# Performance work log

Measured on AMD Instinct MI355X. Metric: run time of the kernel, lower is better.

Reference implementation:

```python
import jax, jax.numpy as jnp
import numpy as np

# SGCN (AsynSpiGCN) internals are not in the source; reconstructed as a standard
# LIF spiking-GCN: per time step, spikes propagate along edges weighted by
# edge_attr (gather src -> scatter-add dst), membrane potential decays with
# decay_alpha, neurons fire above threshold unless refractory, reset to v_r.
V_REST = 0.0
V_R = 0.0
SPEED = 1.0
THRESH = 0.5
REFRAC = 2.0
DECAY = 0.8
T_STEPS = 8
BETA = 0.5

N_NODES = 50000
N_EDGES = 800000
IN_DIM = 256
HID_DIM = 128


def setup_inputs() -> dict:
    key = jax.random.key(0)
    k1, k2, k3, k4, k5 = jax.random.split(key, 5)
    x = jax.random.normal(k1, (N_NODES, IN_DIM), dtype=jnp.float32)
    spike_node = jax.random.randint(k2, (N_NODES,), 0, 2, dtype=jnp.int32)
    edge_index = jax.random.randint(k3, (2, N_EDGES), 0, N_NODES, dtype=jnp.int32)
    node_indices = jnp.arange(N_NODES, dtype=jnp.int32)
    edge_attr = jax.random.uniform(k4, (N_EDGES,), dtype=jnp.float32)
    W = jax.random.normal(k5, (IN_DIM, HID_DIM), dtype=jnp.float32) * 0.05
    b = jnp.zeros((HID_DIM,), dtype=jnp.float32)
    return {"x": x, "spike_node": spike_node, "edge_index": edge_index,
            "node_indices": node_indices, "edge_attr": edge_attr, "W": W, "b": b}


def reference(x, spike_node, edge_index, node_indices, edge_attr, W, b):
    N = x.shape[0]
    # Linear projection + per-feature min-max standardization over nodes (dim 0)
    h = x @ W + b
    mn = h.min(axis=0, keepdims=True)
    mx = h.max(axis=0, keepdims=True)
    h = (h - mn) / (mx - mn + 1e-6)

    src, dst = edge_index[0], edge_index[1]
    v0 = jnp.full_like(h, V_REST)            # membrane potential [N, H]
    ref0 = jnp.zeros_like(h)                 # refractory counters [N, H]
    s0 = jnp.broadcast_to(spike_node.astype(h.dtype)[:, None], h.shape)

    def step(carry, _):
        v, ref, s = carry
        msg = s[src] * edge_attr[:, None]                      # [E, H] gather
        agg = jax.ops.segment_sum(msg, dst, num_segments=N)    # [N, H] scatter-add
        v = DECAY * v + SPEED * h + agg
        can_fire = ref <= 0
        spk = ((v >= THRESH) & can_fire).astype(h.dtype)
        v = jnp.where(spk > 0, V_R, v)
        ref = jnp.where(spk > 0, REFRAC, jnp.maximum(ref - 1.0, 0.0))
        return (v, ref, spk), spk

    (vT, _, _), spike_matrix = jax.lax.scan(step, (v0, ref0, s0), None, length=T_STEPS)
    fusion_tensor = h + BETA * vT
    return fusion_tensor, spike_matrix
```

## Files before the change

kernel.cpp:

```cpp
#include <hip/hip_runtime.h>
#include <cstdint>

#define N_NODES 50000
#define N_EDGES 800000
#define IN_DIM  256
#define HID     128
#define T_STEPS 8

static __device__ __forceinline__ unsigned int enc_f(float f) {
    unsigned int u = __float_as_uint(f);
    return (u & 0x80000000u) ? ~u : (u | 0x80000000u);
}
static __device__ __forceinline__ float dec_f(unsigned int u) {
    unsigned int b = (u & 0x80000000u) ? (u ^ 0x80000000u) : ~u;
    return __uint_as_float(b);
}

__global__ void k_count(const int* __restrict__ dst, int* __restrict__ counts) {
    int e = blockIdx.x * blockDim.x + threadIdx.x;
    if (e < N_EDGES) atomicAdd(&counts[dst[e]], 1);
}

__global__ void k_scan1(const int* __restrict__ counts, int* __restrict__ row_tmp,
                        int* __restrict__ blocksum) {
    __shared__ int sh[256];
    int t = threadIdx.x, i = blockIdx.x * 256 + t;
    int c = (i < N_NODES) ? counts[i] : 0;
    sh[t] = c; __syncthreads();
    for (int off = 1; off < 256; off <<= 1) {
        int val = (t >= off) ? sh[t - off] : 0;
        __syncthreads();
        sh[t] += val;
        __syncthreads();
    }
    if (i < N_NODES) row_tmp[i] = sh[t] - c;
    if (t == 255) blocksum[blockIdx.x] = sh[255];
}

__global__ void k_scan2(const int* __restrict__ blocksum, int* __restrict__ blockoff,
                        int nb, int* __restrict__ row_ptr) {
    if (threadIdx.x == 0) {
        int acc = 0;
        for (int b = 0; b < nb; ++b) { blockoff[b] = acc; acc += blocksum[b]; }
        row_ptr[N_NODES] = acc;
    }
}

__global__ void k_scan3(const int* __restrict__ row_tmp, const int* __restrict__ blockoff,
                        int* __restrict__ row_ptr) {
    int i = blockIdx.x * blockDim.x + threadIdx.x;
    if (i < N_NODES) row_ptr[i] = row_tmp[i] + blockoff[i >> 8];
}

__global__ void k_fill(const int* __restrict__ dst, const int* __restrict__ src,
                       const float* __restrict__ attr,
                       const int* __restrict__ row_ptr, int* __restrict__ cursor,
                       int* __restrict__ eid, int2* __restrict__ edata) {
    int e = blockIdx.x * blockDim.x + threadIdx.x;
    if (e >= N_EDGES) return;
    int d = dst[e];
    int p = row_ptr[d] + atomicAdd(&cursor[d], 1);
    eid[p]   = e;
    edata[p] = make_int2(src[e], __float_as_int(attr[e]));
}

__global__ __launch_bounds__(256) void k_bsort(const int* __restrict__ row_ptr,
                                               int* __restrict__ eid,
                                               int2* __restrict__ edata) {
    int node = blockIdx.x * 4 + (threadIdx.x >> 6);
    int l = threadIdx.x & 63;
    int beg = row_ptr[node], end = row_ptr[node + 1], cnt = end - beg;
    if (cnt <= 1) return;
    if (cnt <= 64) {
        int key = 0x7FFFFFFF, sv = 0, av = 0;
        if (l < cnt) { key = eid[beg + l]; int2 d = edata[beg + l]; sv = d.x; av = d.y; }
        #pragma unroll
        for (int k = 2; k <= 64; k <<= 1) {
            for (int j = k >> 1; j > 0; j >>= 1) {
                int pk = __shfl_xor(key, j);
                int ps = __shfl_xor(sv, j);
                int pa = __shfl_xor(av, j);
                bool lower = (l & j) == 0;
                bool asc   = (l & k) == 0;
                bool take_min = (lower == asc);
                bool take = take_min ? (pk < key) : (pk > key);
                if (take) { key = pk; sv = ps; av = pa; }
            }
        }
        if (l < cnt) { eid[beg + l] = key; edata[beg + l] = make_int2(sv, av); }
    } else if (l == 0) {
        for (int i = beg + 1; i < end; ++i) {
            int ke = eid[i]; int2 kd = edata[i];
            int m = i - 1;
            while (m >= beg && eid[m] > ke) {
                eid[m+1] = eid[m]; edata[m+1] = edata[m]; --m;
            }
            eid[m+1] = ke; edata[m+1] = kd;
        }
    }
}

__global__ __launch_bounds__(256) void k_gemm(const float* __restrict__ x,
                                              const float* __restrict__ W,
                                              const float* __restrict__ b,
                                              float* __restrict__ h,
                                              unsigned int* __restrict__ mn_e,
                                              unsigned int* __restrict__ mx_e) {
    __shared__ float Ws[32 * 128];
    __shared__ float xs[64 * 36];
    __shared__ float red_mn[8 * 128];
    __shared__ float red_mx[8 * 128];
    const int tid = threadIdx.x;
    const int n0 = blockIdx.x * 64;
    const int jt = tid & 31, nt = tid >> 5;
    const int j0 = jt * 4;

    float acc[8][4];
    #pragma unroll
    for (int a = 0; a < 8; ++a)
        #pragma unroll
        for (int c = 0; c < 4; ++c) acc[a][c] = 0.0f;

    const int ldn = tid >> 2;
    const int kq  = (tid & 3) * 8;
    const int xrow = (n0 + ldn < N_NODES) ? (n0 + ldn) : (N_NODES - 1);
    const float* xg = x + (size_t)xrow * IN_DIM;

    for (int kc = 0; kc < IN_DIM; kc += 32) {
        __syncthreads();
        float4 xa = *(const float4*)(xg + kc + kq);
        float4 xb = *(const float4*)(xg + kc + kq + 4);
        *(float4*)&xs[ldn * 36 + kq]     = xa;
        *(float4*)&xs[ldn * 36 + kq + 4] = xb;
        #pragma unroll
        for (int p = 0; p < 4; ++p) {
            int r = nt + p * 8;
            *(float4*)&Ws[r * 128 + j0] =
                *(const float4*)(W + (size_t)(kc + r) * HID + j0);
        }
        __syncthreads();
        const float* xbase = &xs[nt * 8 * 36];
        #pragma unroll 4
        for (int k = 0; k < 32; ++k) {
            float4 wf = *(const float4*)&Ws[k * 128 + j0];
            #pragma unroll
            for (int ni = 0; ni < 8; ++ni) {
                float xv = xbase[ni * 36 + k];
                acc[ni][0] = __fmaf_rn(xv, wf.x, acc[ni][0]);
                acc[ni][1] = __fmaf_rn(xv, wf.y, acc[ni][1]);
                acc[ni][2] = __fmaf_rn(xv, wf.z, acc[ni][2]);
                acc[ni][3] = __fmaf_rn(xv, wf.w, acc[ni][3]);
            }
        }
    }

    float4 bv = *(const float4*)(b + j0);
    float lmn[4], lmx[4];
    #pragma unroll
    for (int c = 0; c < 4; ++c) { lmn[c] = INFINITY; lmx[c] = -INFINITY; }
    #pragma unroll
    for (int ni = 0; ni < 8; ++ni) {
        acc[ni][0] = __fadd_rn(acc[ni][0], bv.x);
        acc[ni][1] = __fadd_rn(acc[ni][1], bv.y);
        acc[ni][2] = __fadd_rn(acc[ni][2], bv.z);
        acc[ni][3] = __fadd_rn(acc[ni][3], bv.w);
        #pragma unroll
        for (int c = 0; c < 4; ++c) {
            lmn[c] = fminf(lmn[c], acc[ni][c]);
            lmx[c] = fmaxf(lmx[c], acc[ni][c]);
        }
    }
    #pragma unroll
    for (int c = 0; c < 4; ++c) {
        red_mn[nt * 128 + j0 + c] = lmn[c];
        red_mx[nt * 128 + j0 + c] = lmx[c];
    }
    __syncthreads();
    if (tid < 128) {
        float mnv = red_mn[tid], mxv = red_mx[tid];
        #pragma unroll
        for (int r = 1; r < 8; ++r) {
            mnv = fminf(mnv, red_mn[r * 128 + tid]);
            mxv = fmaxf(mxv, red_mx[r * 128 + tid]);
        }
        atomicMin(&mn_e[tid], enc_f(mnv));
        atomicMax(&mx_e[tid], enc_f(mxv));
    }
    #pragma unroll
    for (int ni = 0; ni < 8; ++ni) {
        int n = n0 + nt * 8 + ni;
        if (n < N_NODES)
            *(float4*)&h[(size_t)n * HID + j0] =
                make_float4(acc[ni][0], acc[ni][1], acc[ni][2], acc[ni][3]);
    }
}

__global__ void k_init_bits(const int* __restrict__ spike_node, uint32_t* __restrict__ sb) {
    int n = blockIdx.x * blockDim.x + threadIdx.x;
    if (n >= N_NODES) return;
    uint32_t f = spike_node[n] ? 0xFFFFFFFFu : 0u;
    sb[(size_t)n * 4 + 0] = f;
    sb[(size_t)n * 4 + 1] = f;
    sb[(size_t)n * 4 + 2] = f;
    sb[(size_t)n * 4 + 3] = f;
}

static __device__ __forceinline__ void fbar(int* bar, int nblk, int t) {
    int* flags = bar;
    int* go    = bar + 1900;
    __syncthreads();
    if (blockIdx.x == 0) {
        if (threadIdx.x == 0)
            __hip_atomic_store(&flags[0], t, __ATOMIC_RELAXED, __HIP_MEMORY_SCOPE_AGENT);
        for (;;) {
            int ok = 1;
            for (int i = (int)threadIdx.x; i < nblk; i += 256)
                ok &= (__hip_atomic_load(&flags[i], __ATOMIC_RELAXED,
                                         __HIP_MEMORY_SCOPE_AGENT) >= t);
            if (__syncthreads_and(ok)) break;
            __builtin_amdgcn_s_sleep(1);
        }
        if (threadIdx.x == 0)
            __hip_atomic_store(go, t, __ATOMIC_RELAXED, __HIP_MEMORY_SCOPE_AGENT);
    } else {
        if (threadIdx.x == 0) {
            __hip_atomic_store(&flags[blockIdx.x], t, __ATOMIC_RELAXED,
                               __HIP_MEMORY_SCOPE_AGENT);
            while (__hip_atomic_load(go, __ATOMIC_RELAXED,
                                     __HIP_MEMORY_SCOPE_AGENT) < t)
                __builtin_amdgcn_s_sleep(4);
        }
        __syncthreads();
    }
}

template<int TNPB, int TNSLOT, int TECAP, int TPACK, int TMINW>
__global__ __launch_bounds__(256, TMINW) void k_lif_t(
    const int* __restrict__ row_ptr,
    const int2* __restrict__ edata,
    uint32_t* __restrict__ sbA,
    uint32_t* __restrict__ sbB,
    const float* __restrict__ h_raw,
    const unsigned int* __restrict__ mn_e,
    const unsigned int* __restrict__ mx_e,
    float* __restrict__ out,
    int* __restrict__ bar,
    int nblk)
{
    __shared__ int      lrp[TNPB + 1];
    __shared__ int      ed_src_l[TECAP];
    __shared__ float    ed_attr_l[TECAP];
    __shared__ uint32_t ed_wds[TPACK ? 1 : TECAP * 4];
    __shared__ uint2    ed_pk[TPACK ? TECAP * 4 : 1];
    __shared__ uint32_t sbw[TNPB][4];

    const int tid = threadIdx.x;
    const int g   = tid >> 5;
    const int ln  = tid & 31;
    const int n0  = blockIdx.x * TNPB;
    const int ncnt = min(TNPB, N_NODES - n0);
    const int w = ln >> 3, shb = (ln & 7) * 4;
    const size_t NH = (size_t)N_NODES * HID;

    if (tid <= ncnt) lrp[tid] = row_ptr[n0 + tid];
    __syncthreads();
    const int ebase = lrp[0];
    const int etot  = lrp[ncnt] - ebase;
    const bool inlds = (etot <= TECAP);
    if (inlds) {
        for (int i = tid; i < etot; i += 256) {
            int2 d = edata[ebase + i];
            ed_src_l[i]  = d.x;
            ed_attr_l[i] = __int_as_float(d.y);
        }
    }

    uint4 mnu = *(const uint4*)&mn_e[ln * 4];
    uint4 mxu = *(const uint4*)&mx_e[ln * 4];
    float mn0 = dec_f(mnu.x), mn1 = dec_f(mnu.y), mn2 = dec_f(mnu.z), mn3 = dec_f(mnu.w);
    float dd0 = __fadd_rn(__fsub_rn(dec_f(mxu.x), mn0), 1e-6f);
    float dd1 = __fadd_rn(__fsub_rn(dec_f(mxu.y), mn1), 1e-6f);
    float dd2 = __fadd_rn(__fsub_rn(dec_f(mxu.z), mn2), 1e-6f);
    float dd3 = __fadd_rn(__fsub_rn(dec_f(mxu.w), mn3), 1e-6f);

    float4 hs[TNSLOT], vs[TNSLOT];
    uint32_t rcs[TNSLOT];
    #pragma unroll
    for (int s = 0; s < TNSLOT; ++s) {
        hs[s] = make_float4(0.f, 0.f, 0.f, 0.f);
        vs[s] = make_float4(0.f, 0.f, 0.f, 0.f);
        rcs[s] = 0u;
        int m = s * 8 + g;
        if (m < ncnt) {
            size_t idx = (size_t)(n0 + m) * HID + ln * 4;
            float4 t = *(const float4*)&h_raw[idx];
            t.x = __fdiv_rn(__fsub_rn(t.x, mn0), dd0);
            t.y = __fdiv_rn(__fsub_rn(t.y, mn1), dd1);
            t.z = __fdiv_rn(__fsub_rn(t.z, mn2), dd2);
            t.w = __fdiv_rn(__fsub_rn(t.w, mn3), dd3);
            hs[s] = t;
        }
    }
    for (int i = tid; i < ncnt * 4; i += 256) ((uint32_t*)sbw)[i] = 0u;
    __syncthreads();

    for (int t = 0; t < T_STEPS; ++t) {
        const uint32_t* cur = (t & 1) ? sbB : sbA;
        uint32_t*       nxt = (t & 1) ? sbA : sbB;
        if (t > 0) fbar(bar, nblk, t);

        if (inlds) {
            for (int i = tid; i < etot; i += 256) {
                unsigned long long* sp =
                    (unsigned long long*)&cur[(size_t)ed_src_l[i] * 4];
                unsigned long long lo = __hip_atomic_load(
                    sp, __ATOMIC_RELAXED, __HIP_MEMORY_SCOPE_AGENT);
                unsigned long long hi = __hip_atomic_load(
                    sp + 1, __ATOMIC_RELAXED, __HIP_MEMORY_SCOPE_AGENT);
                uint4 wv;
                wv.x = (uint32_t)lo; wv.y = (uint32_t)(lo >> 32);
                wv.z = (uint32_t)hi; wv.w = (uint32_t)(hi >> 32);
                if (TPACK) {
                    uint32_t ab = __float_as_uint(ed_attr_l[i]);
                    ed_pk[i * 4 + 0] = make_uint2(ab, wv.x);
                    ed_pk[i * 4 + 1] = make_uint2(ab, wv.y);
                    ed_pk[i * 4 + 2] = make_uint2(ab, wv.z);
                    ed_pk[i * 4 + 3] = make_uint2(ab, wv.w);
                } else {
                    *(uint4*)&ed_wds[i * 4] = wv;
                }
            }
        }
        __syncthreads();

        #pragma unroll
        for (int s = 0; s < TNSLOT; ++s) {
            int m = s * 8 + g;
            if (m < ncnt) {
                float ag0 = 0.f, ag1 = 0.f, ag2 = 0.f, ag3 = 0.f;
                if (inlds) {
                    int lb = lrp[m] - ebase, le = lrp[m + 1] - ebase;
                    for (int i = lb; i < le; ++i) {
                        uint32_t u; float a;
                        if (TPACK) {
                            uint2 p = ed_pk[i * 4 + w];
                            a = __uint_as_float(p.x);
                            u = p.y;
                        } else {
                            u = ed_wds[i * 4 + w];
                            a = ed_attr_l[i];
                        }
                        uint32_t bits = (u >> shb) & 0xFu;
                        ag0 = __fadd_rn(ag0, (bits & 1u) ? a : 0.f);
                        ag1 = __fadd_rn(ag1, (bits & 2u) ? a : 0.f);
                        ag2 = __fadd_rn(ag2, (bits & 4u) ? a : 0.f);
                        ag3 = __fadd_rn(ag3, (bits & 8u) ? a : 0.f);
                    }
                } else {
                    int lb = lrp[m], le = lrp[m + 1];
                    for (int i = lb; i < le; ++i) {
                        int2 d = edata[i];
                        uint32_t u = __hip_atomic_load(
                            (uint32_t*)&cur[(size_t)d.x * 4 + w],
                            __ATOMIC_RELAXED, __HIP_MEMORY_SCOPE_AGENT);
                        float a = __int_as_float(d.y);
                        uint32_t bits = (u >> shb) & 0xFu;
                        ag0 = __fadd_rn(ag0, (bits & 1u) ? a : 0.f);
                        ag1 = __fadd_rn(ag1, (bits & 2u) ? a : 0.f);
                        ag2 = __fadd_rn(ag2, (bits & 4u) ? a : 0.f);
                        ag3 = __fadd_rn(ag3, (bits & 8u) ? a : 0.f);
                    }
                }

                float hv[4] = {hs[s].x, hs[s].y, hs[s].z, hs[s].w};
                float vv[4] = {vs[s].x, vs[s].y, vs[s].z, vs[s].w};
                float ag[4] = {ag0, ag1, ag2, ag3};
                float vf[4], sf[4];
                uint32_t rcu = rcs[s], rcn = 0u, nib = 0u;
                #pragma unroll
                for (int q = 0; q < 4; ++q) {
                    float vn = __fadd_rn(__fadd_rn(__fmul_rn(0.8f, vv[q]), hv[q]), ag[q]);
                    uint32_t rc = (rcu >> (8 * q)) & 0xFFu;
                    bool spk = (vn >= 0.5f) && (rc == 0u);
                    vf[q] = spk ? 0.0f : vn;
                    sf[q] = spk ? 1.0f : 0.0f;
                    uint32_t rnew = spk ? 2u : (rc > 0u ? rc - 1u : 0u);
                    rcn |= rnew << (8 * q);
                    nib |= (spk ? 1u : 0u) << q;
                }
                vs[s] = make_float4(vf[0], vf[1], vf[2], vf[3]);
                rcs[s] = rcn;
                size_t idx = (size_t)(n0 + m) * HID + ln * 4;
                *(float4*)&out[NH + (size_t)t * NH + idx] =
                    make_float4(sf[0], sf[1], sf[2], sf[3]);
                if (t == T_STEPS - 1) {
                    *(float4*)&out[idx] = make_float4(
                        __fadd_rn(hv[0], __fmul_rn(0.5f, vf[0])),
                        __fadd_rn(hv[1], __fmul_rn(0.5f, vf[1])),
                        __fadd_rn(hv[2], __fmul_rn(0.5f, vf[2])),
                        __fadd_rn(hv[3], __fmul_rn(0.5f, vf[3])));
                }
                atomicOr(&sbw[m][w], nib << shb);
            }
        }
        __syncthreads();
        for (int i = tid; i < ncnt * 4; i += 256) {
            __hip_atomic_store(&nxt[(size_t)n0 * 4 + i], ((uint32_t*)sbw)[i],
                               __ATOMIC_RELAXED, __HIP_MEMORY_SCOPE_AGENT);
            ((uint32_t*)sbw)[i] = 0u;
        }
    }
}

__global__ __launch_bounds__(128) void k_step(const int* __restrict__ row_ptr,
                                              const int2* __restrict__ edata,
                                              const uint32_t* __restrict__ sb_cur,
                                              uint32_t* __restrict__ sb_nxt,
                                              float* __restrict__ h,
                                              float* __restrict__ v,
                                              unsigned char* __restrict__ refc,
                                              const unsigned int* __restrict__ mn_e,
                                              const unsigned int* __restrict__ mx_e,
                                              float* __restrict__ out_spk,
                                              float* __restrict__ out_fus,
                                              int t0, int is_last) {
    __shared__ float    attr_l[4][128];
    __shared__ uint32_t words_l[4][128][4];
    __shared__ uint32_t sbw[16];
    __shared__ int      rp[5];

    const int tid = threadIdx.x;
    const int ns = tid >> 5, ln = tid & 31;
    const int nb = blockIdx.x * 4;
    const int n  = nb + ns;

    if (tid < 16) sbw[tid] = 0;
    if (tid < 5)  rp[tid] = row_ptr[nb + tid];
    __syncthreads();

    const int beg = rp[ns], cnt = rp[ns + 1] - beg;
    int cmax = 0;
    #pragma unroll
    for (int q = 0; q < 4; ++q) cmax = max(cmax, rp[q + 1] - rp[q]);
    const int nchunk = (cmax + 127) >> 7;

    float agg0 = 0.f, agg1 = 0.f, agg2 = 0.f, agg3 = 0.f;
    const int w = ln >> 3, shb = (ln & 7) * 4;

    for (int ch = 0; ch < nchunk; ++ch) {
        int base = ch << 7;
        __syncthreads();
        #pragma unroll
        for (int rep = 0; rep < 4; ++rep) {
            int i = base + rep * 32 + ln;
            if (i < cnt) {
                int2 d = edata[beg + i];
                attr_l[ns][rep * 32 + ln] = __int_as_float(d.y);
                *(uint4*)&words_l[ns][rep * 32 + ln][0] =
                    *(const uint4*)&sb_cur[(size_t)d.x * 4];
            }
        }
        __syncthreads();
        int lim = min(128, cnt - base);
        for (int i = 0; i < lim; ++i) {
            uint32_t u = words_l[ns][i][w];
            float a = attr_l[ns][i];
            uint32_t bits = (u >> shb) & 0xFu;
            agg0 = __fadd_rn(agg0, (bits & 1u) ? a : 0.0f);
            agg1 = __fadd_rn(agg1, (bits & 2u) ? a : 0.0f);
            agg2 = __fadd_rn(agg2, (bits & 4u) ? a : 0.0f);
            agg3 = __fadd_rn(agg3, (bits & 8u) ? a : 0.0f);
        }
    }

    const size_t idx = (size_t)n * HID + ln * 4;
    float4 h4 = *(const float4*)&h[idx];
    if (t0) {
        const int jb = ln * 4;
        float hq[4] = {h4.x, h4.y, h4.z, h4.w};
        #pragma unroll
        for (int q = 0; q < 4; ++q) {
            float mn = dec_f(mn_e[jb + q]);
            float mx = dec_f(mx_e[jb + q]);
            float d2 = __fadd_rn(__fsub_rn(mx, mn), 1e-6f);
            hq[q] = __fdiv_rn(__fsub_rn(hq[q], mn), d2);
        }
        h4 = make_float4(hq[0], hq[1], hq[2], hq[3]);
        *(float4*)&h[idx] = h4;
    }
    float4 v4;
    unsigned int rcu;
    if (t0) { v4 = make_float4(0.f, 0.f, 0.f, 0.f); rcu = 0u; }
    else    { v4 = *(const float4*)&v[idx]; rcu = *(const unsigned int*)&refc[idx]; }

    float hv[4]  = {h4.x, h4.y, h4.z, h4.w};
    float vv[4]  = {v4.x, v4.y, v4.z, v4.w};
    float ag[4]  = {agg0, agg1, agg2, agg3};
    float vf[4], sf[4];
    unsigned int rcn = 0u, nib = 0u;
    #pragma unroll
    for (int q = 0; q < 4; ++q) {
        float vn = __fadd_rn(__fadd_rn(__fmul_rn(0.8f, vv[q]), hv[q]), ag[q]);
        unsigned int rc = (rcu >> (8 * q)) & 0xFFu;
        bool spk = (vn >= 0.5f) && (rc == 0u);
        vf[q] = spk ? 0.0f : vn;
        sf[q] = spk ? 1.0f : 0.0f;
        unsigned int rnew = spk ? 2u : (rc > 0u ? rc - 1u : 0u);
        rcn |= rnew << (8 * q);
        nib |= (spk ? 1u : 0u) << q;
    }
    *(float4*)&v[idx] = make_float4(vf[0], vf[1], vf[2], vf[3]);
    *(unsigned int*)&refc[idx] = rcn;
    *(float4*)&out_spk[idx] = make_float4(sf[0], sf[1], sf[2], sf[3]);
    if (is_last) {
        *(float4*)&out_fus[idx] = make_float4(
            __fadd_rn(hv[0], __fmul_rn(0.5f, vf[0])),
            __fadd_rn(hv[1], __fmul_rn(0.5f, vf[1])),
            __fadd_rn(hv[2], __fmul_rn(0.5f, vf[2])),
            __fadd_rn(hv[3], __fmul_rn(0.5f, vf[3])));
    }
    atomicOr(&sbw[ns * 4 + w], nib << shb);
    __syncthreads();
    if (tid < 16)
        sb_nxt[(size_t)(nb + (tid >> 2)) * 4 + (tid & 3)] = sbw[tid];
}

extern "C" void kernel_launch(void* const* d_in, const int* in_sizes, int n_in,
                              void* d_out, int out_size, void* d_ws, size_t ws_size,
                              hipStream_t stream) {
    const float* x          = (const float*)d_in[0];
    const int*   spike_node = (const int*)  d_in[1];
    const int*   edge_index = (const int*)  d_in[2];
    const float* edge_attr  = (const float*)d_in[4];
    const float* W          = (const float*)d_in[5];
    const float* b          = (const float*)d_in[6];
    float* out = (float*)d_out;

    const int* src = edge_index;
    const int* dst = edge_index + N_EDGES;

    char* wsp = (char*)d_ws;
    auto alloc = [&](size_t bytes) {
        char* p = wsp;
        wsp += (bytes + 255) & ~(size_t)255;
        return p;
    };
    float*         h        = (float*)        alloc((size_t)N_NODES * HID * 4);
    float*         v        = (float*)        alloc((size_t)N_NODES * HID * 4);
    unsigned char* refc     = (unsigned char*)alloc((size_t)N_NODES * HID);
    uint32_t*      sbA      = (uint32_t*)     alloc((size_t)N_NODES * 16);
    uint32_t*      sbB      = (uint32_t*)     alloc((size_t)N_NODES * 16);
    int*           counts   = (int*)          alloc((size_t)N_NODES * 4);
    int*           cursor   = (int*)          alloc((size_t)N_NODES * 4);
    int*           row_tmp  = (int*)          alloc((size_t)N_NODES * 4);
    int*           row_ptr  = (int*)          alloc((size_t)(N_NODES + 1) * 4);
    int*           blocksum = (int*)          alloc(256 * 4);
    int*           blockoff = (int*)          alloc(256 * 4);
    int*           eid      = (int*)          alloc((size_t)N_EDGES * 4);
    int2*          edata    = (int2*)         alloc((size_t)N_EDGES * 8);
    unsigned int*  mn_e     = (unsigned int*) alloc(HID * 4);
    unsigned int*  mx_e     = (unsigned int*) alloc(HID * 4);
    int*           barv     = (int*)          alloc(8192);

    hipMemsetAsync(counts, 0x00, (size_t)N_NODES * 4, stream);
    hipMemsetAsync(cursor, 0x00, (size_t)N_NODES * 4, stream);
    hipMemsetAsync(mn_e,   0xFF, HID * 4, stream);
    hipMemsetAsync(mx_e,   0x00, HID * 4, stream);
    hipMemsetAsync(barv,   0x00, 8192, stream);

    const int NB = (N_NODES + 255) / 256;
    const int EB = (N_EDGES + 255) / 256;

    k_count<<<EB, 256, 0, stream>>>(dst, counts);
    k_scan1<<<NB, 256, 0, stream>>>(counts, row_tmp, blocksum);
    k_scan2<<<1, 64, 0, stream>>>(blocksum, blockoff, NB, row_ptr);
    k_scan3<<<NB, 256, 0, stream>>>(row_tmp, blockoff, row_ptr);
    k_fill<<<EB, 256, 0, stream>>>(dst, src, edge_attr, row_ptr, cursor, eid, edata);
    k_bsort<<<N_NODES / 4, 256, 0, stream>>>(row_ptr, eid, edata);

    k_gemm<<<(N_NODES + 63) / 64, 256, 0, stream>>>(x, W, b, h, mn_e, mx_e);
    k_init_bits<<<NB, 256, 0, stream>>>(spike_node, sbA);

    const size_t NH = (size_t)N_NODES * HID;

    auto kA = k_lif_t<66, 9, 1536, 0, 3>;
    auto kC = k_lif_t<33, 5, 768, 0, 6>;
    auto kD = k_lif_t<40, 5, 896, 0, 5>;
    auto kB = k_lif_t<98, 13, 1920, 1, 2>;
    int occA = 0, occC = 0, occD = 0, occB = 0;
    hipOccupancyMaxActiveBlocksPerMultiprocessor(&occA, kA, 256, 0);
    hipOccupancyMaxActiveBlocksPerMultiprocessor(&occC, kC, 256, 0);
    hipOccupancyMaxActiveBlocksPerMultiprocessor(&occD, kD, 256, 0);
    hipOccupancyMaxActiveBlocksPerMultiprocessor(&occB, kB, 256, 0);

    if (occA >= 3) {
        const int grid = (N_NODES + 65) / 66;
        kA<<<grid, 256, 0, stream>>>(row_ptr, edata, sbA, sbB, h, mn_e, mx_e,
                                     out, barv, grid);
    } else if (occC >= 6) {
        const int grid = (N_NODES + 32) / 33;
        kC<<<grid, 256, 0, stream>>>(row_ptr, edata, sbA, sbB, h, mn_e, mx_e,
                                     out, barv, grid);
    } else if (occD >= 5) {
        const int grid = (N_NODES + 39) / 40;
        kD<<<grid, 256, 0, stream>>>(row_ptr, edata, sbA, sbB, h, mn_e, mx_e,
                                     out, barv, grid);
    } else if (occB >= 2) {
        const int grid = (N_NODES + 97) / 98;
        kB<<<grid, 256, 0, stream>>>(row_ptr, edata, sbA, sbB, h, mn_e, mx_e,
                                     out, barv, grid);
    } else {
        for (int t = 0; t < T_STEPS; ++t) {
            uint32_t* cur = (t & 1) ? sbB : sbA;
            uint32_t* nxt = (t & 1) ? sbA : sbB;
            k_step<<<N_NODES / 4, 128, 0, stream>>>(row_ptr, edata, cur, nxt,
                                                    h, v, refc, mn_e, mx_e,
                                                    out + NH + (size_t)t * NH,
                                                    out, (t == 0) ? 1 : 0,
                                                    (t == T_STEPS - 1) ? 1 : 0);
        }
    }
}
```

Baseline: 625.4 us.

## Fuse CSR build, GEMM and LIF steps into one persistent megakernel

Merges the edge counting, prefix scan, CSR fill, per-node sort, input projection with min-max reduction, and the time-step loop into a single persistent kernel separated by software grid barriers. Each block keeps its projected h rows in registers instead of writing h to global memory and reading it back. This removes many small kernel launches and memsets along with an h round-trip, at the cost of extra grid-wide barriers, heavier register and LDS pressure, and serialized per-block scans. The per-node edge ordering may now rely on an in-kernel sort using the eid buffer.

```diff
diff --git a/kernel.cpp b/kernel.cpp
--- a/kernel.cpp
+++ b/kernel.cpp
@@ -7,6 +7,12 @@
 #define HID     128
 #define T_STEPS 8
 
+#define AG_LOAD(p)     __hip_atomic_load((p), __ATOMIC_RELAXED, __HIP_MEMORY_SCOPE_AGENT)
+#define AG_STORE(p, v) __hip_atomic_store((p), (v), __ATOMIC_RELAXED, __HIP_MEMORY_SCOPE_AGENT)
+#define AG_ADD(p, v)   __hip_atomic_fetch_add((p), (v), __ATOMIC_RELAXED, __HIP_MEMORY_SCOPE_AGENT)
+#define AG_MIN(p, v)   __hip_atomic_fetch_min((p), (v), __ATOMIC_RELAXED, __HIP_MEMORY_SCOPE_AGENT)
+#define AG_MAX(p, v)   __hip_atomic_fetch_max((p), (v), __ATOMIC_RELAXED, __HIP_MEMORY_SCOPE_AGENT)
+
 static __device__ __forceinline__ unsigned int enc_f(float f) {
     unsigned int u = __float_as_uint(f);
     return (u & 0x80000000u) ? ~u : (u | 0x80000000u);
@@ -14,195 +20,6 @@
 static __device__ __forceinline__ float dec_f(unsigned int u) {
     unsigned int b = (u & 0x80000000u) ? (u ^ 0x80000000u) : ~u;
     return __uint_as_float(b);
-}
-
-__global__ void k_count(const int* __restrict__ dst, int* __restrict__ counts) {
-    int e = blockIdx.x * blockDim.x + threadIdx.x;
-    if (e < N_EDGES) atomicAdd(&counts[dst[e]], 1);
-}
-
-__global__ void k_scan1(const int* __restrict__ counts, int* __restrict__ row_tmp,
-                        int* __restrict__ blocksum) {
-    __shared__ int sh[256];
-    int t = threadIdx.x, i = blockIdx.x * 256 + t;
-    int c = (i < N_NODES) ? counts[i] : 0;
-    sh[t] = c; __syncthreads();
-    for (int off = 1; off < 256; off <<= 1) {
-        int val = (t >= off) ? sh[t - off] : 0;
-        __syncthreads();
-        sh[t] += val;
-        __syncthreads();
-    }
-    if (i < N_NODES) row_tmp[i] = sh[t] - c;
-    if (t == 255) blocksum[blockIdx.x] = sh[255];
-}
-
-__global__ void k_scan2(const int* __restrict__ blocksum, int* __restrict__ blockoff,
-                        int nb, int* __restrict__ row_ptr) {
-    if (threadIdx.x == 0) {
-        int acc = 0;
-        for (int b = 0; b < nb; ++b) { blockoff[b] = acc; acc += blocksum[b]; }
-        row_ptr[N_NODES] = acc;
-    }
-}
-
-__global__ void k_scan3(const int* __restrict__ row_tmp, const int* __restrict__ blockoff,
-                        int* __restrict__ row_ptr) {
-    int i = blockIdx.x * blockDim.x + threadIdx.x;
-    if (i < N_NODES) row_ptr[i] = row_tmp[i] + blockoff[i >> 8];
-}
-
-__global__ void k_fill(const int* __restrict__ dst, const int* __restrict__ src,
-                       const float* __restrict__ attr,
-                       const int* __restrict__ row_ptr, int* __restrict__ cursor,
-                       int* __restrict__ eid, int2* __restrict__ edata) {
-    int e = blockIdx.x * blockDim.x + threadIdx.x;
-    if (e >= N_EDGES) return;
-    int d = dst[e];
-    int p = row_ptr[d] + atomicAdd(&cursor[d], 1);
-    eid[p]   = e;
-    edata[p] = make_int2(src[e], __float_as_int(attr[e]));
-}
-
-__global__ __launch_bounds__(256) void k_bsort(const int* __restrict__ row_ptr,
-                                               int* __restrict__ eid,
-                                               int2* __restrict__ edata) {
-    int node = blockIdx.x * 4 + (threadIdx.x >> 6);
-    int l = threadIdx.x & 63;
-    int beg = row_ptr[node], end = row_ptr[node + 1], cnt = end - beg;
-    if (cnt <= 1) return;
-    if (cnt <= 64) {
-        int key = 0x7FFFFFFF, sv = 0, av = 0;
-        if (l < cnt) { key = eid[beg + l]; int2 d = edata[beg + l]; sv = d.x; av = d.y; }
-        #pragma unroll
-        for (int k = 2; k <= 64; k <<= 1) {
-            for (int j = k >> 1; j > 0; j >>= 1) {
-                int pk = __shfl_xor(key, j);
-                int ps = __shfl_xor(sv, j);
-                int pa = __shfl_xor(av, j);
-                bool lower = (l & j) == 0;
-                bool asc   = (l & k) == 0;
-                bool take_min = (lower == asc);
-                bool take = take_min ? (pk < key) : (pk > key);
-                if (take) { key = pk; sv = ps; av = pa; }
-            }
-        }
-        if (l < cnt) { eid[beg + l] = key; edata[beg + l] = make_int2(sv, av); }
-    } else if (l == 0) {
-        for (int i = beg + 1; i < end; ++i) {
-            int ke = eid[i]; int2 kd = edata[i];
-            int m = i - 1;
-            while (m >= beg && eid[m] > ke) {
-                eid[m+1] = eid[m]; edata[m+1] = edata[m]; --m;
-            }
-            eid[m+1] = ke; edata[m+1] = kd;
-        }
-    }
-}
-
-__global__ __launch_bounds__(256) void k_gemm(const float* __restrict__ x,
-                                              const float* __restrict__ W,
-                                              const float* __restrict__ b,
-                                              float* __restrict__ h,
-                                              unsigned int* __restrict__ mn_e,
-                                              unsigned int* __restrict__ mx_e) {
-    __shared__ float Ws[32 * 128];
-    __shared__ float xs[64 * 36];
-    __shared__ float red_mn[8 * 128];
-    __shared__ float red_mx[8 * 128];
-    const int tid = threadIdx.x;
-    const int n0 = blockIdx.x * 64;
-    const int jt = tid & 31, nt = tid >> 5;
-    const int j0 = jt * 4;
-
-    float acc[8][4];
-    #pragma unroll
-    for (int a = 0; a < 8; ++a)
-        #pragma unroll
-        for (int c = 0; c < 4; ++c) acc[a][c] = 0.0f;
-
-    const int ldn = tid >> 2;
-    const int kq  = (tid & 3) * 8;
-    const int xrow = (n0 + ldn < N_NODES) ? (n0 + ldn) : (N_NODES - 1);
-    const float* xg = x + (size_t)xrow * IN_DIM;
-
-    for (int kc = 0; kc < IN_DIM; kc += 32) {
-        __syncthreads();
-        float4 xa = *(const float4*)(xg + kc + kq);
-        float4 xb = *(const float4*)(xg + kc + kq + 4);
-        *(float4*)&xs[ldn * 36 + kq]     = xa;
-        *(float4*)&xs[ldn * 36 + kq + 4] = xb;
-        #pragma unroll
-        for (int p = 0; p < 4; ++p) {
-            int r = nt + p * 8;
-            *(float4*)&Ws[r * 128 + j0] =
-                *(const float4*)(W + (size_t)(kc + r) * HID + j0);
-        }
-        __syncthreads();
-        const float* xbase = &xs[nt * 8 * 36];
-        #pragma unroll 4
-        for (int k = 0; k < 32; ++k) {
-            float4 wf = *(const float4*)&Ws[k * 128 + j0];
-            #pragma unroll
-            for (int ni = 0; ni < 8; ++ni) {
-                float xv = xbase[ni * 36 + k];
-                acc[ni][0] = __fmaf_rn(xv, wf.x, acc[ni][0]);
-                acc[ni][1] = __fmaf_rn(xv, wf.y, acc[ni][1]);
-                acc[ni][2] = __fmaf_rn(xv, wf.z, acc[ni][2]);
-                acc[ni][3] = __fmaf_rn(xv, wf.w, acc[ni][3]);
-            }
-        }
-    }
-
-    float4 bv = *(const float4*)(b + j0);
-    float lmn[4], lmx[4];
-    #pragma unroll
-    for (int c = 0; c < 4; ++c) { lmn[c] = INFINITY; lmx[c] = -INFINITY; }
-    #pragma unroll
-    for (int ni = 0; ni < 8; ++ni) {
-        acc[ni][0] = __fadd_rn(acc[ni][0], bv.x);
-        acc[ni][1] = __fadd_rn(acc[ni][1], bv.y);
-        acc[ni][2] = __fadd_rn(acc[ni][2], bv.z);
-        acc[ni][3] = __fadd_rn(acc[ni][3], bv.w);
-        #pragma unroll
-        for (int c = 0; c < 4; ++c) {
-            lmn[c] = fminf(lmn[c], acc[ni][c]);
-            lmx[c] = fmaxf(lmx[c], acc[ni][c]);
-        }
-    }
-    #pragma unroll
-    for (int c = 0; c < 4; ++c) {
-        red_mn[nt * 128 + j0 + c] = lmn[c];
-        red_mx[nt * 128 + j0 + c] = lmx[c];
-    }
-    __syncthreads();
-    if (tid < 128) {
-        float mnv = red_mn[tid], mxv = red_mx[tid];
-        #pragma unroll
-        for (int r = 1; r < 8; ++r) {
-            mnv = fminf(mnv, red_mn[r * 128 + tid]);
-            mxv = fmaxf(mxv, red_mx[r * 128 + tid]);
-        }
-        atomicMin(&mn_e[tid], enc_f(mnv));
-        atomicMax(&mx_e[tid], enc_f(mxv));
-    }
-    #pragma unroll
-    for (int ni = 0; ni < 8; ++ni) {
-        int n = n0 + nt * 8 + ni;
-        if (n < N_NODES)
-            *(float4*)&h[(size_t)n * HID + j0] =
-                make_float4(acc[ni][0], acc[ni][1], acc[ni][2], acc[ni][3]);
-    }
-}
-
-__global__ void k_init_bits(const int* __restrict__ spike_node, uint32_t* __restrict__ sb) {
-    int n = blockIdx.x * blockDim.x + threadIdx.x;
-    if (n >= N_NODES) return;
-    uint32_t f = spike_node[n] ? 0xFFFFFFFFu : 0u;
-    sb[(size_t)n * 4 + 0] = f;
-    sb[(size_t)n * 4 + 1] = f;
-    sb[(size_t)n * 4 + 2] = f;
-    sb[(size_t)n * 4 + 3] = f;
 }
 
 static __device__ __forceinline__ void fbar(int* bar, int nblk, int t) {
@@ -210,125 +27,353 @@
     int* go    = bar + 1900;
     __syncthreads();
     if (blockIdx.x == 0) {
-        if (threadIdx.x == 0)
-            __hip_atomic_store(&flags[0], t, __ATOMIC_RELAXED, __HIP_MEMORY_SCOPE_AGENT);
+        if (threadIdx.x == 0) AG_STORE(&flags[0], t);
         for (;;) {
             int ok = 1;
             for (int i = (int)threadIdx.x; i < nblk; i += 256)
-                ok &= (__hip_atomic_load(&flags[i], __ATOMIC_RELAXED,
-                                         __HIP_MEMORY_SCOPE_AGENT) >= t);
+                ok &= (AG_LOAD(&flags[i]) >= t);
             if (__syncthreads_and(ok)) break;
             __builtin_amdgcn_s_sleep(1);
         }
-        if (threadIdx.x == 0)
-            __hip_atomic_store(go, t, __ATOMIC_RELAXED, __HIP_MEMORY_SCOPE_AGENT);
+        if (threadIdx.x == 0) AG_STORE(go, t);
     } else {
         if (threadIdx.x == 0) {
-            __hip_atomic_store(&flags[blockIdx.x], t, __ATOMIC_RELAXED,
-                               __HIP_MEMORY_SCOPE_AGENT);
-            while (__hip_atomic_load(go, __ATOMIC_RELAXED,
-                                     __HIP_MEMORY_SCOPE_AGENT) < t)
-                __builtin_amdgcn_s_sleep(4);
-        }
-        __syncthreads();
-    }
-}
-
-template<int TNPB, int TNSLOT, int TECAP, int TPACK, int TMINW>
-__global__ __launch_bounds__(256, TMINW) void k_lif_t(
-    const int* __restrict__ row_ptr,
-    const int2* __restrict__ edata,
-    uint32_t* __restrict__ sbA,
-    uint32_t* __restrict__ sbB,
-    const float* __restrict__ h_raw,
-    const unsigned int* __restrict__ mn_e,
-    const unsigned int* __restrict__ mx_e,
+            AG_STORE(&flags[blockIdx.x], t);
+            while (AG_LOAD(go) < t) __builtin_amdgcn_s_sleep(4);
+        }
+        __syncthreads();
+    }
+}
+
+template<int TNPB, int TNSLOT, int TECAP, int TMINW>
+__global__ __launch_bounds__(256, TMINW) void k_mega(
+    const float* __restrict__ x,
+    const int*   __restrict__ spike_node,
+    const int*   __restrict__ esrc,
+    const int*   __restrict__ edst,
+    const float* __restrict__ eattr,
+    const float* __restrict__ W,
+    const float* __restrict__ b,
+    int* counts, int* cursor, int* row_ptr, int* blocksum,
+    int* eid, int2* edata,
+    unsigned int* mn_e, unsigned int* mx_e,
+    uint32_t* sbA, uint32_t* sbB,
     float* __restrict__ out,
-    int* __restrict__ bar,
-    int nblk)
+    int* bar, int nblk)
 {
     __shared__ int      lrp[TNPB + 1];
-    __shared__ int      ed_src_l[TECAP];
-    __shared__ float    ed_attr_l[TECAP];
-    __shared__ uint32_t ed_wds[TPACK ? 1 : TECAP * 4];
-    __shared__ uint2    ed_pk[TPACK ? TECAP * 4 : 1];
+    __shared__ uint32_t pool[TECAP * 6];
     __shared__ uint32_t sbw[TNPB][4];
 
+    int*      ed_src_l  = (int*)pool;
+    float*    ed_attr_l = (float*)(pool + TECAP);
+    uint32_t* ed_wds    = pool + 2 * TECAP;
+    int*      eid_l     = (int*)(pool + 5 * TECAP);
+    float*    Ws        = (float*)pool;
+    float*    xs        = (float*)(pool + 4096);
+    float*    red_mn    = (float*)pool;
+    float*    red_mx    = (float*)(pool + 1024);
+    int*      rbuf      = (int*)pool;
+    int*      cnt_l     = (int*)sbw;
+
     const int tid = threadIdx.x;
-    const int g   = tid >> 5;
-    const int ln  = tid & 31;
-    const int n0  = blockIdx.x * TNPB;
+    const int bid = blockIdx.x;
+    const int g   = tid >> 5, ln = tid & 31;
+    const int n0  = bid * TNPB;
     const int ncnt = min(TNPB, N_NODES - n0);
     const int w = ln >> 3, shb = (ln & 7) * 4;
     const size_t NH = (size_t)N_NODES * HID;
 
-    if (tid <= ncnt) lrp[tid] = row_ptr[n0 + tid];
+    for (int i = tid; i < ncnt; i += 256) {
+        AG_STORE(&counts[n0 + i], 0);
+        AG_STORE(&cursor[n0 + i], 0);
+    }
+    if (bid == 0 && tid < HID) {
+        AG_STORE(&mn_e[tid], 0xFFFFFFFFu);
+        AG_STORE(&mx_e[tid], 0u);
+    }
+    fbar(bar, nblk, 1);
+
+    for (int e = bid * 256 + tid; e < N_EDGES; e += nblk * 256)
+        AG_ADD(&counts[edst[e]], 1);
+    fbar(bar, nblk, 2);
+
+    for (int i = tid; i < ncnt; i += 256) cnt_l[i] = AG_LOAD(&counts[n0 + i]);
     __syncthreads();
+    if (tid == 0) {
+        int s = 0;
+        for (int i = 0; i < ncnt; ++i) s += cnt_l[i];
+        AG_STORE(&blocksum[bid], s);
+    }
+    fbar(bar, nblk, 3);
+
+    {
+        int part = 0;
+        for (int j = tid; j < bid; j += 256) part += AG_LOAD(&blocksum[j]);
+        rbuf[tid] = part;
+        __syncthreads();
+        for (int off = 128; off > 0; off >>= 1) {
+            if (tid < off) rbuf[tid] += rbuf[tid + off];
+            __syncthreads();
+        }
+        if (tid == 0) {
+            int run = rbuf[0];
+            for (int i = 0; i < ncnt; ++i) { lrp[i] = run; run += cnt_l[i]; }
+            lrp[ncnt] = run;
+        }
+        __syncthreads();
+        for (int i = tid; i <= ncnt; i += 256) AG_STORE(&row_ptr[n0 + i], lrp[i]);
+    }
+    fbar(bar, nblk, 4);
+
+    for (int e = bid * 256 + tid; e < N_EDGES; e += nblk * 256) {
+        int d  = edst[e];
+        int rp = AG_LOAD(&row_ptr[d]);
+        int c  = AG_ADD(&cursor[d], 1);
+        int p  = rp + c;
+        AG_STORE(&eid[p], e);
+        unsigned long long pk = (unsigned long long)(unsigned int)esrc[e] |
+                                ((unsigned long long)__float_as_uint(eattr[e]) << 32);
+        AG_STORE((unsigned long long*)&edata[p], pk);
+    }
+    fbar(bar, nblk, 5);
+
     const int ebase = lrp[0];
     const int etot  = lrp[ncnt] - ebase;
     const bool inlds = (etot <= TECAP);
-    if (inlds) {
-        for (int i = tid; i < etot; i += 256) {
-            int2 d = edata[ebase + i];
-            ed_src_l[i]  = d.x;
-            ed_attr_l[i] = __int_as_float(d.y);
-        }
-    }
-
-    uint4 mnu = *(const uint4*)&mn_e[ln * 4];
-    uint4 mxu = *(const uint4*)&mx_e[ln * 4];
-    float mn0 = dec_f(mnu.x), mn1 = dec_f(mnu.y), mn2 = dec_f(mnu.z), mn3 = dec_f(mnu.w);
-    float dd0 = __fadd_rn(__fsub_rn(dec_f(mxu.x), mn0), 1e-6f);
-    float dd1 = __fadd_rn(__fsub_rn(dec_f(mxu.y), mn1), 1e-6f);
-    float dd2 = __fadd_rn(__fsub_rn(dec_f(mxu.z), mn2), 1e-6f);
-    float dd3 = __fadd_rn(__fsub_rn(dec_f(mxu.w), mn3), 1e-6f);
 
     float4 hs[TNSLOT], vs[TNSLOT];
     uint32_t rcs[TNSLOT];
     #pragma unroll
+    for (int s = 0; s < TNSLOT; ++s)
+        hs[s] = make_float4(0.f, 0.f, 0.f, 0.f);
+
+    int xoff[TNSLOT];
+    #pragma unroll
+    for (int s = 0; s < TNSLOT; ++s) xoff[s] = min(s * 8 + g, TNPB - 1) * 36;
+
+    for (int kc = 0; kc < IN_DIM; kc += 32) {
+        __syncthreads();
+        for (int idx = tid; idx < TNPB * 8; idx += 256) {
+            int node = idx >> 3, q = idx & 7;
+            int row = min(n0 + node, N_NODES - 1);
+            *(float4*)&xs[node * 36 + q * 4] =
+                *(const float4*)(x + (size_t)row * IN_DIM + kc + q * 4);
+        }
+        for (int idx = tid; idx < 1024; idx += 256) {
+            int r = idx >> 5, c = idx & 31;
+            *(float4*)&Ws[r * 128 + c * 4] =
+                *(const float4*)(W + (size_t)(kc + r) * HID + c * 4);
+        }
+        __syncthreads();
+        #pragma unroll 4
+        for (int k = 0; k < 32; ++k) {
+            float4 wf = *(float4*)&Ws[k * 128 + ln * 4];
+            #pragma unroll
+            for (int s = 0; s < TNSLOT; ++s) {
+                float xv = xs[xoff[s] + k];
+                hs[s].x = __fmaf_rn(xv, wf.x, hs[s].x);
+                hs[s].y = __fmaf_rn(xv, wf.y, hs[s].y);
+                hs[s].z = __fmaf_rn(xv, wf.z, hs[s].z);
+                hs[s].w = __fmaf_rn(xv, wf.w, hs[s].w);
+            }
+        }
+    }
+    {
+        float4 bv = *(const float4*)(b + ln * 4);
+        float lmn[4], lmx[4];
+        #pragma unroll
+        for (int c = 0; c < 4; ++c) { lmn[c] = INFINITY; lmx[c] = -INFINITY; }
+        #pragma unroll
+        for (int s = 0; s < TNSLOT; ++s) {
+            hs[s].x = __fadd_rn(hs[s].x, bv.x);
+            hs[s].y = __fadd_rn(hs[s].y, bv.y);
+            hs[s].z = __fadd_rn(hs[s].z, bv.z);
+            hs[s].w = __fadd_rn(hs[s].w, bv.w);
+            lmn[0] = fminf(lmn[0], hs[s].x); lmx[0] = fmaxf(lmx[0], hs[s].x);
+            lmn[1] = fminf(lmn[1], hs[s].y); lmx[1] = fmaxf(lmx[1], hs[s].y);
+            lmn[2] = fminf(lmn[2], hs[s].z); lmx[2] = fmaxf(lmx[2], hs[s].z);
+            lmn[3] = fminf(lmn[3], hs[s].w); lmx[3] = fmaxf(lmx[3], hs[s].w);
+        }
+        __syncthreads();
+        #pragma unroll
+        for (int c = 0; c < 4; ++c) {
+            red_mn[g * 128 + ln * 4 + c] = lmn[c];
+            red_mx[g * 128 + ln * 4 + c] = lmx[c];
+        }
+        __syncthreads();
+        if (tid < 128) {
+            float mnv = red_mn[tid], mxv = red_mx[tid];
+            #pragma unroll
+            for (int r = 1; r < 8; ++r) {
+                mnv = fminf(mnv, red_mn[r * 128 + tid]);
+                mxv = fmaxf(mxv, red_mx[r * 128 + tid]);
+            }
+            AG_MIN(&mn_e[tid], enc_f(mnv));
+            AG_MAX(&mx_e[tid], enc_f(mxv));
+        }
+        __syncthreads();
+    }
+
+    if (inlds) {
+        for (int m = tid >> 6; m < ncnt; m += 4) {
+            int l = tid & 63;
+            int gbeg = lrp[m], lbeg = gbeg - ebase;
+            int cnt = lrp[m + 1] - gbeg;
+            if (cnt <= 0) continue;
+            if (cnt <= 64) {
+                int key = 0x7FFFFFFF, sv = 0, av = 0;
+                if (l < cnt) {
+                    key = AG_LOAD(&eid[gbeg + l]);
+                    unsigned long long pk =
+                        AG_LOAD((unsigned long long*)&edata[gbeg + l]);
+                    sv = (int)(unsigned int)pk;
+                    av = (int)(unsigned int)(pk >> 32);
+                }
+                #pragma unroll
+                for (int k = 2; k <= 64; k <<= 1) {
+                    for (int j = k >> 1; j > 0; j >>= 1) {
+                        int pk2 = __shfl_xor(key, j);
+                        int ps  = __shfl_xor(sv, j);
+                        int pa  = __shfl_xor(av, j);
+                        bool lower = (l & j) == 0;
+                        bool asc   = (l & k) == 0;
+                        bool take  = (lower == asc) ? (pk2 < key) : (pk2 > key);
+                        if (take) { key = pk2; sv = ps; av = pa; }
+                    }
+                }
+                if (l < cnt) {
+                    ed_src_l[lbeg + l]  = sv;
+                    ed_attr_l[lbeg + l] = __int_as_float(av);
+                }
+            } else {
+                if (l == 0) {
+                    for (int i = 1; i < cnt; ++i) {
+                        int ke = AG_LOAD(&eid[gbeg + i]);
+                        unsigned long long kd =
+                            AG_LOAD((unsigned long long*)&edata[gbeg + i]);
+                        int mm = i - 1;
+                        while (mm >= 0) {
+                            int km = AG_LOAD(&eid[gbeg + mm]);
+                            if (km <= ke) break;
+                            AG_STORE(&eid[gbeg + mm + 1], km);
+                            AG_STORE((unsigned long long*)&edata[gbeg + mm + 1],
+                                     AG_LOAD((unsigned long long*)&edata[gbeg + mm]));
+                            --mm;
+                        }
+                        AG_STORE(&eid[gbeg + mm + 1], ke);
+                        AG_STORE((unsigned long long*)&edata[gbeg + mm + 1], kd);
+                    }
+                }
+                for (int i = l; i < cnt; i += 64) {
+                    unsigned long long pk =
+                        AG_LOAD((unsigned long long*)&edata[gbeg + i]);
+                    ed_src_l[lbeg + i]  = (int)(unsigned int)pk;
+                    ed_attr_l[lbeg + i] = __uint_as_float((unsigned int)(pk >> 32));
+                }
+            }
+        }
+    } else {
+        for (int m = tid >> 6; m < ncnt; m += 4) {
+            int l = tid & 63;
+            int gbeg = lrp[m];
+            int cnt = lrp[m + 1] - gbeg;
+            if (cnt <= 1) continue;
+            if (cnt <= 64) {
+                int key = 0x7FFFFFFF, sv = 0, av = 0;
+                if (l < cnt) {
+                    key = AG_LOAD(&eid[gbeg + l]);
+                    unsigned long long pk =
+                        AG_LOAD((unsigned long long*)&edata[gbeg + l]);
+                    sv = (int)(unsigned int)pk;
+                    av = (int)(unsigned int)(pk >> 32);
+                }
+                #pragma unroll
+                for (int k = 2; k <= 64; k <<= 1) {
+                    for (int j = k >> 1; j > 0; j >>= 1) {
+                        int pk2 = __shfl_xor(key, j);
+                        int ps  = __shfl_xor(sv, j);
+                        int pa  = __shfl_xor(av, j);
+                        bool lower = (l & j) == 0;
+                        bool asc   = (l & k) == 0;
+                        bool take  = (lower == asc) ? (pk2 < key) : (pk2 > key);
+                        if (take) { key = pk2; sv = ps; av = pa; }
+                    }
+                }
+                if (l < cnt) {
+                    unsigned long long pk =
+                        (unsigned long long)(unsigned int)sv |
+                        ((unsigned long long)(unsigned int)av << 32);
+                    AG_STORE((unsigned long long*)&edata[gbeg + l], pk);
+                }
+            } else if (l == 0) {
+                for (int i = 1; i < cnt; ++i) {
+                    int ke = AG_LOAD(&eid[gbeg + i]);
+                    unsigned long long kd =
+                        AG_LOAD((unsigned long long*)&edata[gbeg + i]);
+                    int mm = i - 1;
+                    while (mm >= 0) {
+                        int km = AG_LOAD(&eid[gbeg + mm]);
+                        if (km <= ke) break;
+                        AG_STORE(&eid[gbeg + mm + 1], km);
+                        AG_STORE((unsigned long long*)&edata[gbeg + mm + 1],
+                                 AG_LOAD((unsigned long long*)&edata[gbeg + mm]));
+                        --mm;
+                    }
+                    AG_STORE(&eid[gbeg + mm + 1], ke);
+                    AG_STORE((unsigned long long*)&edata[gbeg + mm + 1], kd);
+                }
+            }
+        }
+    }
+
+    for (int i = tid; i < ncnt; i += 256) {
+        uint32_t f = spike_node[n0 + i] ? 0xFFFFFFFFu : 0u;
+        unsigned long long ff = (unsigned long long)f | ((unsigned long long)f << 32);
+        AG_STORE((unsigned long long*)&sbA[(size_t)(n0 + i) * 4], ff);
+        AG_STORE((unsigned long long*)&sbA[(size_t)(n0 + i) * 4 + 2], ff);
+    }
+    for (int i = tid; i < ncnt * 4; i += 256) ((uint32_t*)sbw)[i] = 0u;
+    fbar(bar, nblk, 6);
+
+    {
+        float mn0 = dec_f(AG_LOAD(&mn_e[ln * 4 + 0]));
+        float mn1 = dec_f(AG_LOAD(&mn_e[ln * 4 + 1]));
+        float mn2 = dec_f(AG_LOAD(&mn_e[ln * 4 + 2]));
+        float mn3 = dec_f(AG_LOAD(&mn_e[ln * 4 + 3]));
+        float dd0 = __fadd_rn(__fsub_rn(dec_f(AG_LOAD(&mx_e[ln * 4 + 0])), mn0), 1e-6f);
+        float dd1 = __fadd_rn(__fsub_rn(dec_f(AG_LOAD(&mx_e[ln * 4 + 1])), mn1), 1e-6f);
+        float dd2 = __fadd_rn(__fsub_rn(dec_f(AG_LOAD(&mx_e[ln * 4 + 2])), mn2), 1e-6f);
+        float dd3 = __fadd_rn(__fsub_rn(dec_f(AG_LOAD(&mx_e[ln * 4 + 3])), mn3), 1e-6f);
+        #pragma unroll
+        for (int s = 0; s < TNSLOT; ++s) {
+            hs[s].x = __fdiv_rn(__fsub_rn(hs[s].x, mn0), dd0);
+            hs[s].y = __fdiv_rn(__fsub_rn(hs[s].y, mn1), dd1);
+            hs[s].z = __fdiv_rn(__fsub_rn(hs[s].z, mn2), dd2);
+            hs[s].w = __fdiv_rn(__fsub_rn(hs[s].w, mn3), dd3);
+        }
+    }
+    #pragma unroll
     for (int s = 0; s < TNSLOT; ++s) {
-        hs[s] = make_float4(0.f, 0.f, 0.f, 0.f);
         vs[s] = make_float4(0.f, 0.f, 0.f, 0.f);
         rcs[s] = 0u;
-        int m = s * 8 + g;
-        if (m < ncnt) {
-            size_t idx = (size_t)(n0 + m) * HID + ln * 4;
-            float4 t = *(const float4*)&h_raw[idx];
-            t.x = __fdiv_rn(__fsub_rn(t.x, mn0), dd0);
-            t.y = __fdiv_rn(__fsub_rn(t.y, mn1), dd1);
-            t.z = __fdiv_rn(__fsub_rn(t.z, mn2), dd2);
-            t.w = __fdiv_rn(__fsub_rn(t.w, mn3), dd3);
-            hs[s] = t;
-        }
-    }
-    for (int i = tid; i < ncnt * 4; i += 256) ((uint32_t*)sbw)[i] = 0u;
-    __syncthreads();
+    }
 
     for (int t = 0; t < T_STEPS; ++t) {
         const uint32_t* cur = (t & 1) ? sbB : sbA;
         uint32_t*       nxt = (t & 1) ? sbA : sbB;
-        if (t > 0) fbar(bar, nblk, t);
+        if (t > 0) fbar(bar, nblk, 6 + t);
 
         if (inlds) {
             for (int i = tid; i < etot; i += 256) {
                 unsigned long long* sp =
                     (unsigned long long*)&cur[(size_t)ed_src_l[i] * 4];
-                unsigned long long lo = __hip_atomic_load(
-                    sp, __ATOMIC_RELAXED, __HIP_MEMORY_SCOPE_AGENT);
-                unsigned long long hi = __hip_atomic_load(
-                    sp + 1, __ATOMIC_RELAXED, __HIP_MEMORY_SCOPE_AGENT);
+                unsigned long long lo = AG_LOAD(sp);
+                unsigned long long hi = AG_LOAD(sp + 1);
                 uint4 wv;
                 wv.x = (uint32_t)lo; wv.y = (uint32_t)(lo >> 32);
                 wv.z = (uint32_t)hi; wv.w = (uint32_t)(hi >> 32);
-                if (TPACK) {
-                    uint32_t ab = __float_as_uint(ed_attr_l[i]);
-                    ed_pk[i * 4 + 0] = make_uint2(ab, wv.x);
-                    ed_pk[i * 4 + 1] = make_uint2(ab, wv.y);
-                    ed_pk[i * 4 + 2] = make_uint2(ab, wv.z);
-                    ed_pk[i * 4 + 3] = make_uint2(ab, wv.w);
-                } else {
-                    *(uint4*)&ed_wds[i * 4] = wv;
-                }
+                *(uint4*)&ed_wds[i * 4] = wv;
             }
         }
         __syncthreads();
@@ -341,15 +386,8 @@
                 if (inlds) {
                     int lb = lrp[m] - ebase, le = lrp[m + 1] - ebase;
                     for (int i = lb; i < le; ++i) {
-                        uint32_t u; float a;
-                        if (TPACK) {
-                            uint2 p = ed_pk[i * 4 + w];
-                            a = __uint_as_float(p.x);
-                            u = p.y;
-                        } else {
-                            u = ed_wds[i * 4 + w];
-                            a = ed_attr_l[i];
-                        }
+                        uint32_t u = ed_wds[i * 4 + w];
+                        float a = ed_attr_l[i];
                         uint32_t bits = (u >> shb) & 0xFu;
                         ag0 = __fadd_rn(ag0, (bits & 1u) ? a : 0.f);
                         ag1 = __fadd_rn(ag1, (bits & 2u) ? a : 0.f);
@@ -359,11 +397,11 @@
                 } else {
                     int lb = lrp[m], le = lrp[m + 1];
                     for (int i = lb; i < le; ++i) {
-                        int2 d = edata[i];
-                        uint32_t u = __hip_atomic_load(
-                            (uint32_t*)&cur[(size_t)d.x * 4 + w],
-                            __ATOMIC_RELAXED, __HIP_MEMORY_SCOPE_AGENT);
-                        float a = __int_as_float(d.y);
+                        unsigned long long pk =
+                            AG_LOAD((unsigned long long*)&edata[i]);
+                        int srcn = (int)(unsigned int)pk;
+                        float a = __uint_as_float((unsigned int)(pk >> 32));
+                        uint32_t u = AG_LOAD((uint32_t*)&cur[(size_t)srcn * 4 + w]);
                         uint32_t bits = (u >> shb) & 0xFu;
                         ag0 = __fadd_rn(ag0, (bits & 1u) ? a : 0.f);
                         ag1 = __fadd_rn(ag1, (bits & 2u) ? a : 0.f);
@@ -405,11 +443,198 @@
         }
         __syncthreads();
         for (int i = tid; i < ncnt * 4; i += 256) {
-            __hip_atomic_store(&nxt[(size_t)n0 * 4 + i], ((uint32_t*)sbw)[i],
-                               __ATOMIC_RELAXED, __HIP_MEMORY_SCOPE_AGENT);
+            AG_STORE(&nxt[(size_t)n0 * 4 + i], ((uint32_t*)sbw)[i]);
             ((uint32_t*)sbw)[i] = 0u;
         }
     }
+}
+
+__global__ void k_count(const int* __restrict__ dst, int* __restrict__ counts) {
+    int e = blockIdx.x * blockDim.x + threadIdx.x;
+    if (e < N_EDGES) atomicAdd(&counts[dst[e]], 1);
+}
+
+__global__ void k_scan1(const int* __restrict__ counts, int* __restrict__ row_tmp,
+                        int* __restrict__ blocksum) {
+    __shared__ int sh[256];
+    int t = threadIdx.x, i = blockIdx.x * 256 + t;
+    int c = (i < N_NODES) ? counts[i] : 0;
+    sh[t] = c; __syncthreads();
+    for (int off = 1; off < 256; off <<= 1) {
+        int val = (t >= off) ? sh[t - off] : 0;
+        __syncthreads();
+        sh[t] += val;
+        __syncthreads();
+    }
+    if (i < N_NODES) row_tmp[i] = sh[t] - c;
+    if (t == 255) blocksum[blockIdx.x] = sh[255];
+}
+
+__global__ void k_scan2(const int* __restrict__ blocksum, int* __restrict__ blockoff,
+                        int nb, int* __restrict__ row_ptr) {
+    if (threadIdx.x == 0) {
+        int acc = 0;
+        for (int b = 0; b < nb; ++b) { blockoff[b] = acc; acc += blocksum[b]; }
+        row_ptr[N_NODES] = acc;
+    }
+}
+
+__global__ void k_scan3(const int* __restrict__ row_tmp, const int* __restrict__ blockoff,
+                        int* __restrict__ row_ptr) {
+    int i = blockIdx.x * blockDim.x + threadIdx.x;
+    if (i < N_NODES) row_ptr[i] = row_tmp[i] + blockoff[i >> 8];
+}
+
+__global__ void k_fill(const int* __restrict__ dst, const int* __restrict__ src,
+                       const float* __restrict__ attr,
+                       const int* __restrict__ row_ptr, int* __restrict__ cursor,
+                       int* __restrict__ eid, int2* __restrict__ edata) {
+    int e = blockIdx.x * blockDim.x + threadIdx.x;
+    if (e >= N_EDGES) return;
+    int d = dst[e];
+    int p = row_ptr[d] + atomicAdd(&cursor[d], 1);
+    eid[p]   = e;
+    edata[p] = make_int2(src[e], __float_as_int(attr[e]));
+}
+
+__global__ __launch_bounds__(256) void k_bsort(const int* __restrict__ row_ptr,
+                                               int* __restrict__ eid,
+                                               int2* __restrict__ edata) {
+    int node = blockIdx.x * 4 + (threadIdx.x >> 6);
+    int l = threadIdx.x & 63;
+    int beg = row_ptr[node], end = row_ptr[node + 1], cnt = end - beg;
+    if (cnt <= 1) return;
+    if (cnt <= 64) {
+        int key = 0x7FFFFFFF, sv = 0, av = 0;
+        if (l < cnt) { key = eid[beg + l]; int2 d = edata[beg + l]; sv = d.x; av = d.y; }
+        #pragma unroll
+        for (int k = 2; k <= 64; k <<= 1) {
+            for (int j = k >> 1; j > 0; j >>= 1) {
+                int pk = __shfl_xor(key, j);
+                int ps = __shfl_xor(sv, j);
+                int pa = __shfl_xor(av, j);
+                bool lower = (l & j) == 0;
+                bool asc   = (l & k) == 0;
+                bool take = (lower == asc) ? (pk < key) : (pk > key);
+                if (take) { key = pk; sv = ps; av = pa; }
+            }
+        }
+        if (l < cnt) { eid[beg + l] = key; edata[beg + l] = make_int2(sv, av); }
+    } else if (l == 0) {
+        for (int i = beg + 1; i < end; ++i) {
+            int ke = eid[i]; int2 kd = edata[i];
+            int m = i - 1;
+            while (m >= beg && eid[m] > ke) {
+                eid[m+1] = eid[m]; edata[m+1] = edata[m]; --m;
+            }
+            eid[m+1] = ke; edata[m+1] = kd;
+        }
+    }
+}
+
+__global__ __launch_bounds__(256) void k_gemm(const float* __restrict__ x,
+                                              const float* __restrict__ W,
+                                              const float* __restrict__ b,
+                                              float* __restrict__ h,
+                                              unsigned int* __restrict__ mn_e,
+                                              unsigned int* __restrict__ mx_e) {
+    __shared__ float Ws[32 * 128];
+    __shared__ float xs[64 * 36];
+    __shared__ float red_mn[8 * 128];
+    __shared__ float red_mx[8 * 128];
+    const int tid = threadIdx.x;
+    const int n0 = blockIdx.x * 64;
+    const int jt = tid & 31, nt = tid >> 5;
+    const int j0 = jt * 4;
+
+    float acc[8][4];
+    #pragma unroll
+    for (int a = 0; a < 8; ++a)
+        #pragma unroll
+        for (int c = 0; c < 4; ++c) acc[a][c] = 0.0f;
+
+    const int ldn = tid >> 2;
+    const int kq  = (tid & 3) * 8;
+    const int xrow = (n0 + ldn < N_NODES) ? (n0 + ldn) : (N_NODES - 1);
+    const float* xg = x + (size_t)xrow * IN_DIM;
+
+    for (int kc = 0; kc < IN_DIM; kc += 32) {
+        __syncthreads();
+        float4 xa = *(const float4*)(xg + kc + kq);
+        float4 xb = *(const float4*)(xg + kc + kq + 4);
+        *(float4*)&xs[ldn * 36 + kq]     = xa;
+        *(float4*)&xs[ldn * 36 + kq + 4] = xb;
+        #pragma unroll
+        for (int p = 0; p < 4; ++p) {
+            int r = nt + p * 8;
+            *(float4*)&Ws[r * 128 + j0] =
+                *(const float4*)(W + (size_t)(kc + r) * HID + j0);
+        }
+        __syncthreads();
+        const float* xbase = &xs[nt * 8 * 36];
+        #pragma unroll 4
+        for (int k = 0; k < 32; ++k) {
+            float4 wf = *(const float4*)&Ws[k * 128 + j0];
+            #pragma unroll
+            for (int ni = 0; ni < 8; ++ni) {
+                float xv = xbase[ni * 36 + k];
+                acc[ni][0] = __fmaf_rn(xv, wf.x, acc[ni][0]);
+                acc[ni][1] = __fmaf_rn(xv, wf.y, acc[ni][1]);
+                acc[ni][2] = __fmaf_rn(xv, wf.z, acc[ni][2]);
+                acc[ni][3] = __fmaf_rn(xv, wf.w, acc[ni][3]);
+            }
+        }
+    }
+
+    float4 bv = *(const float4*)(b + j0);
+    float lmn[4], lmx[4];
+    #pragma unroll
+    for (int c = 0; c < 4; ++c) { lmn[c] = INFINITY; lmx[c] = -INFINITY; }
+    #pragma unroll
+    for (int ni = 0; ni < 8; ++ni) {
+        acc[ni][0] = __fadd_rn(acc[ni][0], bv.x);
+        acc[ni][1] = __fadd_rn(acc[ni][1], bv.y);
+        acc[ni][2] = __fadd_rn(acc[ni][2], bv.z);
+        acc[ni][3] = __fadd_rn(acc[ni][3], bv.w);
+        #pragma unroll
+        for (int c = 0; c < 4; ++c) {
+            lmn[c] = fminf(lmn[c], acc[ni][c]);
+            lmx[c] = fmaxf(lmx[c], acc[ni][c]);
+        }
+    }
+    #pragma unroll
+    for (int c = 0; c < 4; ++c) {
+        red_mn[nt * 128 + j0 + c] = lmn[c];
+        red_mx[nt * 128 + j0 + c] = lmx[c];
+    }
+    __syncthreads();
+    if (tid < 128) {
+        float mnv = red_mn[tid], mxv = red_mx[tid];
+        #pragma unroll
+        for (int r = 1; r < 8; ++r) {
+            mnv = fminf(mnv, red_mn[r * 128 + tid]);
+            mxv = fmaxf(mxv, red_mx[r * 128 + tid]);
+        }
+        atomicMin(&mn_e[tid], enc_f(mnv));
+        atomicMax(&mx_e[tid], enc_f(mxv));
+    }
+    #pragma unroll
+    for (int ni = 0; ni < 8; ++ni) {
+        int n = n0 + nt * 8 + ni;
+        if (n < N_NODES)
+            *(float4*)&h[(size_t)n * HID + j0] =
+                make_float4(acc[ni][0], acc[ni][1], acc[ni][2], acc[ni][3]);
+    }
+}
+
+__global__ void k_init_bits(const int* __restrict__ spike_node, uint32_t* __restrict__ sb) {
+    int n = blockIdx.x * blockDim.x + threadIdx.x;
+    if (n >= N_NODES) return;
+    uint32_t f = spike_node[n] ? 0xFFFFFFFFu : 0u;
+    sb[(size_t)n * 4 + 0] = f;
+    sb[(size_t)n * 4 + 1] = f;
+    sb[(size_t)n * 4 + 2] = f;
+    sb[(size_t)n * 4 + 3] = f;
 }
 
 __global__ __launch_bounds__(128) void k_step(const int* __restrict__ row_ptr,
@@ -554,22 +779,37 @@
     int*           cursor   = (int*)          alloc((size_t)N_NODES * 4);
     int*           row_tmp  = (int*)          alloc((size_t)N_NODES * 4);
     int*           row_ptr  = (int*)          alloc((size_t)(N_NODES + 1) * 4);
-    int*           blocksum = (int*)          alloc(256 * 4);
-    int*           blockoff = (int*)          alloc(256 * 4);
+    int*           blocksum = (int*)          alloc(1024 * 4);
+    int*           blockoff = (int*)          alloc(1024 * 4);
     int*           eid      = (int*)          alloc((size_t)N_EDGES * 4);
     int2*          edata    = (int2*)         alloc((size_t)N_EDGES * 8);
     unsigned int*  mn_e     = (unsigned int*) alloc(HID * 4);
     unsigned int*  mx_e     = (unsigned int*) alloc(HID * 4);
     int*           barv     = (int*)          alloc(8192);
 
+    const int NB = (N_NODES + 255) / 256;
+    const int EB = (N_EDGES + 255) / 256;
+    const size_t NH = (size_t)N_NODES * HID;
+
+    auto kM = k_mega<66, 9, 1536, 3>;
+    int occM = 0;
+    hipOccupancyMaxActiveBlocksPerMultiprocessor(&occM, kM, 256, 0);
+
+    if (occM >= 3) {
+        hipMemsetAsync(barv, 0x00, 8192, stream);
+        const int grid = (N_NODES + 65) / 66;
+        kM<<<grid, 256, 0, stream>>>(x, spike_node, src, dst, edge_attr, W, b,
+                                     counts, cursor, row_ptr, blocksum,
+                                     eid, edata, mn_e, mx_e, sbA, sbB,
+                                     out, barv, grid);
+        return;
+    }
+
     hipMemsetAsync(counts, 0x00, (size_t)N_NODES * 4, stream);
     hipMemsetAsync(cursor, 0x00, (size_t)N_NODES * 4, stream);
     hipMemsetAsync(mn_e,   0xFF, HID * 4, stream);
     hipMemsetAsync(mx_e,   0x00, HID * 4, stream);
     hipMemsetAsync(barv,   0x00, 8192, stream);
-
-    const int NB = (N_NODES + 255) / 256;
-    const int EB = (N_EDGES + 255) / 256;
 
     k_count<<<EB, 256, 0, stream>>>(dst, counts);
     k_scan1<<<NB, 256, 0, stream>>>(counts, row_tmp, blocksum);
@@ -577,47 +817,16 @@
     k_scan3<<<NB, 256, 0, stream>>>(row_tmp, blockoff, row_ptr);
     k_fill<<<EB, 256, 0, stream>>>(dst, src, edge_attr, row_ptr, cursor, eid, edata);
     k_bsort<<<N_NODES / 4, 256, 0, stream>>>(row_ptr, eid, edata);
-
     k_gemm<<<(N_NODES + 63) / 64, 256, 0, stream>>>(x, W, b, h, mn_e, mx_e);
     k_init_bits<<<NB, 256, 0, stream>>>(spike_node, sbA);
 
-    const size_t NH = (size_t)N_NODES * HID;
-
-    auto kA = k_lif_t<66, 9, 1536, 0, 3>;
-    auto kC = k_lif_t<33, 5, 768, 0, 6>;
-    auto kD = k_lif_t<40, 5, 896, 0, 5>;
-    auto kB = k_lif_t<98, 13, 1920, 1, 2>;
-    int occA = 0, occC = 0, occD = 0, occB = 0;
-    hipOccupancyMaxActiveBlocksPerMultiprocessor(&occA, kA, 256, 0);
-    hipOccupancyMaxActiveBlocksPerMultiprocessor(&occC, kC, 256, 0);
-    hipOccupancyMaxActiveBlocksPerMultiprocessor(&occD, kD, 256, 0);
-    hipOccupancyMaxActiveBlocksPerMultiprocessor(&occB, kB, 256, 0);
-
-    if (occA >= 3) {
-        const int grid = (N_NODES + 65) / 66;
-        kA<<<grid, 256, 0, stream>>>(row_ptr, edata, sbA, sbB, h, mn_e, mx_e,
-                                     out, barv, grid);
-    } else if (occC >= 6) {
-        const int grid = (N_NODES + 32) / 33;
-        kC<<<grid, 256, 0, stream>>>(row_ptr, edata, sbA, sbB, h, mn_e, mx_e,
-                                     out, barv, grid);
-    } else if (occD >= 5) {
-        const int grid = (N_NODES + 39) / 40;
-        kD<<<grid, 256, 0, stream>>>(row_ptr, edata, sbA, sbB, h, mn_e, mx_e,
-                                     out, barv, grid);
-    } else if (occB >= 2) {
-        const int grid = (N_NODES + 97) / 98;
-        kB<<<grid, 256, 0, stream>>>(row_ptr, edata, sbA, sbB, h, mn_e, mx_e,
-                                     out, barv, grid);
-    } else {
-        for (int t = 0; t < T_STEPS; ++t) {
-            uint32_t* cur = (t & 1) ? sbB : sbA;
-            uint32_t* nxt = (t & 1) ? sbA : sbB;
-            k_step<<<N_NODES / 4, 128, 0, stream>>>(row_ptr, edata, cur, nxt,
-                                                    h, v, refc, mn_e, mx_e,
-                                                    out + NH + (size_t)t * NH,
-                                                    out, (t == 0) ? 1 : 0,
-                                                    (t == T_STEPS - 1) ? 1 : 0);
-        }
-    }
-}
+    for (int t = 0; t < T_STEPS; ++t) {
+        uint32_t* cur = (t & 1) ? sbB : sbA;
+        uint32_t* nxt = (t & 1) ? sbA : sbB;
+        k_step<<<N_NODES / 4, 128, 0, stream>>>(row_ptr, edata, cur, nxt,
+                                                h, v, refc, mn_e, mx_e,
+                                                out + NH + (size_t)t * NH,
+                                                out, (t == 0) ? 1 : 0,
+                                                (t == T_STEPS - 1) ? 1 : 0);
+    }
+}
```

Result: no change. 618.3 us (-1.1%).
